# Optimization experiments

Measured on AMD Instinct MI355X. Metric: run time of the kernel, lower is better.

Reference implementation:

```python
import jax, jax.numpy as jnp
import numpy as np

V, E, H, L, T, B = 50257, 1024, 16, 12, 128, 16
FF = 4 * E
STD = 0.02


def setup_inputs() -> dict:
    key = jax.random.key(0)
    ks = jax.random.split(key, 20)
    n = lambda k, shape: (jax.random.normal(k, shape, dtype=jnp.float32) * STD)
    inp = {
        'idx': jax.random.randint(ks[0], (B, T), 0, V, dtype=jnp.int64),
        'targets': jax.random.randint(ks[1], (B, T), 0, V, dtype=jnp.int64),
        'tok_emb': n(ks[2], (V, E)),
        'pos_emb': n(ks[3], (T, E)),
        'wq': n(ks[4], (L, E, E)),
        'wk': n(ks[5], (L, E, E)),
        'wv': n(ks[6], (L, E, E)),
        'w_proj': n(ks[7], (L, E, E)),
        'b_proj': jnp.zeros((L, E), jnp.float32),
        'ln1_g': jnp.ones((L, E), jnp.float32),
        'ln1_b': jnp.zeros((L, E), jnp.float32),
        'ln2_g': jnp.ones((L, E), jnp.float32),
        'ln2_b': jnp.zeros((L, E), jnp.float32),
        'w_fc1': n(ks[8], (L, E, FF)),
        'b_fc1': jnp.zeros((L, FF), jnp.float32),
        'w_fc2': n(ks[9], (L, FF, E)),
        'b_fc2': jnp.zeros((L, E), jnp.float32),
        'lnf_g': jnp.ones((E,), jnp.float32),
        'lnf_b': jnp.zeros((E,), jnp.float32),
        'w_head': n(ks[10], (E, V)),
        'b_head': jnp.zeros((V,), jnp.float32),
    }
    return inp


def _layernorm(x, g, b, eps=1e-5):
    m = x.mean(-1, keepdims=True)
    v = ((x - m) ** 2).mean(-1, keepdims=True)
    return (x - m) / jnp.sqrt(v + eps) * g + b


def _forward(idx, targets, tok_emb, pos_emb, wq, wk, wv, w_proj, b_proj,
             ln1_g, ln1_b, ln2_g, ln2_b, w_fc1, b_fc1, w_fc2, b_fc2,
             lnf_g, lnf_b, w_head, b_head):
    Bb, Tt = idx.shape
    x = tok_emb[idx] + pos_emb[:Tt]  # (B, T, E)
    causal = jnp.tril(jnp.ones((Tt, Tt), dtype=bool))
    scale = E ** (-0.5)  # NOTE: original scales by full n_embd, not head_size

    def block(x, p):
        (wq_l, wk_l, wv_l, wp_l, bp_l, g1, b1, g2, b2, wf1, bf1, wf2, bf2) = p
        h = _layernorm(x, g1, b1)
        q = (h @ wq_l).reshape(Bb, Tt, H, -1)
        k = (h @ wk_l).reshape(Bb, Tt, H, -1)
        v = (h @ wv_l).reshape(Bb, Tt, H, -1)
        sc = jnp.einsum('bthd,bshd->bhts', q, k) * scale
        sc = jnp.where(causal, sc, -jnp.inf)
        att = jax.nn.softmax(sc, axis=-1)
        o = jnp.einsum('bhts,bshd->bthd', att, v).reshape(Bb, Tt, E)
        x = x + o @ wp_l + bp_l
        h2 = _layernorm(x, g2, b2)
        x = x + jax.nn.relu(h2 @ wf1 + bf1) @ wf2 + bf2
        return x, None

    x, _ = jax.lax.scan(block, x, (wq, wk, wv, w_proj, b_proj, ln1_g, ln1_b,
                                   ln2_g, ln2_b, w_fc1, b_fc1, w_fc2, b_fc2))
    x = _layernorm(x, lnf_g, lnf_b)
    logits = x @ w_head + b_head  # (B, T, V)
    logp = jax.nn.log_softmax(logits, axis=-1)
    nll = -jnp.take_along_axis(logp.reshape(Bb * Tt, -1),
                               targets.reshape(-1, 1), axis=1)
    loss = nll.mean()
    return logits, loss


def reference(idx, targets, tok_emb, pos_emb, wq, wk, wv, w_proj, b_proj,
              ln1_g, ln1_b, ln2_g, ln2_b, w_fc1, b_fc1, w_fc2, b_fc2,
              lnf_g, lnf_b, w_head, b_head):
    return _forward(idx, targets, tok_emb, pos_emb, wq, wk, wv, w_proj, b_proj,
                    ln1_g, ln1_b, ln2_g, ln2_b, w_fc1, b_fc1, w_fc2, b_fc2,
                    lnf_g, lnf_b, w_head, b_head)
```

## Files before the change

kernel.cpp:

```cpp
#include <hip/hip_runtime.h>
#include <math.h>

typedef unsigned short u16;
typedef float f32x4 __attribute__((ext_vector_type(4)));
typedef short bf16x8 __attribute__((ext_vector_type(8)));
typedef unsigned short us4 __attribute__((ext_vector_type(4)));

#define DEVI __device__ __forceinline__

DEVI float bf2f(u16 u) { return __uint_as_float(((unsigned int)u) << 16); }
DEVI u16 f2bf(float f) {
    unsigned int u = __float_as_uint(f);
    u += 0x7fffu + ((u >> 16) & 1u);
    return (u16)(u >> 16);
}

__global__ __launch_bounds__(256) void k_embed(const int* __restrict__ idx,
                                               const float* __restrict__ te,
                                               const float* __restrict__ pe,
                                               float* __restrict__ x) {
    int m = blockIdx.x;
    int t = m & 127;
    int tok = idx[m];
    const f32x4* a = (const f32x4*)(te + (long)tok * 1024);
    const f32x4* p = (const f32x4*)(pe + (long)t * 1024);
    f32x4* o = (f32x4*)(x + (long)m * 1024);
    o[threadIdx.x] = a[threadIdx.x] + p[threadIdx.x];
}

__global__ __launch_bounds__(256) void k_ln(const float* __restrict__ x,
                                            const float* __restrict__ g,
                                            const float* __restrict__ b,
                                            u16* __restrict__ out) {
    __shared__ float red[8];
    int tid = threadIdx.x, lane = tid & 63, wid = tid >> 6;
    int r = blockIdx.x;
    f32x4 v = ((const f32x4*)(x + (long)r * 1024))[tid];
    float s = v.x + v.y + v.z + v.w;
#pragma unroll
    for (int o2 = 32; o2; o2 >>= 1) s += __shfl_xor(s, o2);
    if (lane == 0) red[wid] = s;
    __syncthreads();
    float mean = (red[0] + red[1] + red[2] + red[3]) * (1.0f / 1024.0f);
    f32x4 d; d.x = v.x - mean; d.y = v.y - mean; d.z = v.z - mean; d.w = v.w - mean;
    float sq = d.x * d.x + d.y * d.y + d.z * d.z + d.w * d.w;
#pragma unroll
    for (int o2 = 32; o2; o2 >>= 1) sq += __shfl_xor(sq, o2);
    if (lane == 0) red[4 + wid] = sq;
    __syncthreads();
    float rstd = rsqrtf((red[4] + red[5] + red[6] + red[7]) * (1.0f / 1024.0f) + 1e-5f);
    f32x4 gg = ((const f32x4*)g)[tid];
    f32x4 bb = ((const f32x4*)b)[tid];
    us4 o4;
    o4.x = f2bf(d.x * rstd * gg.x + bb.x);
    o4.y = f2bf(d.y * rstd * gg.y + bb.y);
    o4.z = f2bf(d.z * rstd * gg.z + bb.z);
    o4.w = f2bf(d.w * rstd * gg.w + bb.w);
    ((us4*)(out + (long)r * 1024))[tid] = o4;
}

DEVI void tr_tile(const float* __restrict__ in, u16* __restrict__ out,
                  int K, int N, int k0, int n0, int tid, float (*tile)[65]) {
    int trow = tid >> 4;
    int tcol = (tid & 15) * 4;
#pragma unroll
    for (int p = 0; p < 4; ++p) {
        int k = k0 + trow + p * 16;
        const float* src = in + (long)k * N + n0 + tcol;
#pragma unroll
        for (int j = 0; j < 4; ++j) {
            int n = n0 + tcol + j;
            tile[trow + p * 16][tcol + j] = (n < N) ? src[j] : 0.0f;
        }
    }
    __syncthreads();
#pragma unroll
    for (int p = 0; p < 4; ++p) {
        int n = n0 + trow + p * 16;
        if (n < N) {
            us4 o4;
#pragma unroll
            for (int j = 0; j < 4; ++j) o4[j] = f2bf(tile[tcol + j][trow + p * 16]);
            *(us4*)(out + (long)n * K + k0 + tcol) = o4;
        }
    }
}

__global__ __launch_bounds__(256) void k_tr_one(const float* __restrict__ in,
                                                u16* __restrict__ out, int K, int N) {
    __shared__ float tile[64][65];
    tr_tile(in, out, K, N, blockIdx.y * 64, blockIdx.x * 64, threadIdx.x, tile);
}

__global__ __launch_bounds__(256) void k_tr_layer(
    const float* __restrict__ wq, const float* __restrict__ wk,
    const float* __restrict__ wv, const float* __restrict__ wp,
    const float* __restrict__ f1, const float* __restrict__ f2,
    u16* __restrict__ oqkv, u16* __restrict__ oproj,
    u16* __restrict__ of1, u16* __restrict__ of2) {
    __shared__ float tile[64][65];
    int id = blockIdx.x;
    const float* in; u16* out; int K, N, txx, tyy;
    if (id < 1024) {
        int t = id >> 8, s2 = id & 255;
        txx = s2 & 15; tyy = s2 >> 4; K = 1024; N = 1024;
        in = (t == 0) ? wq : (t == 1) ? wk : (t == 2) ? wv : wp;
        out = (t == 3) ? oproj : oqkv + (long)t * 1024 * 1024;
    } else if (id < 2048) {
        int s2 = id - 1024;
        txx = s2 & 63; tyy = s2 >> 6; K = 1024; N = 4096; in = f1; out = of1;
    } else {
        int s2 = id - 2048;
        txx = s2 & 15; tyy = s2 >> 4; K = 4096; N = 1024; in = f2; out = of2;
    }
    tr_tile(in, out, K, N, tyy * 64, txx * 64, threadIdx.x, tile);
}

template <int ROWS>
DEVI void stage_tile(const u16* __restrict__ g, long row0, long rowmax, int ld,
                     int col0, char* lds, int tid) {
    constexpr int NCH = ROWS * 8;
#pragma unroll
    for (int p = 0; p < NCH / 256; ++p) {
        int c = tid + p * 256;
        int row = c >> 3;
        int gslot = c & 7;
        int gdata = gslot ^ (row & 7);
        long gr = row0 + row;
        if (gr > rowmax) gr = rowmax;
        const u16* src = g + gr * (long)ld + col0 + gdata * 8;
        char* dst = lds + ((long)((tid & 192) + p * 256)) * 16;
        __builtin_amdgcn_global_load_lds(
            (const __attribute__((address_space(1))) void*)src,
            (__attribute__((address_space(3))) void*)dst, 16, 0, 0);
    }
}

template <int BN, bool OUT_BF16, bool RELU, bool HAS_BIAS, bool HAS_RES>
__global__ __launch_bounds__(256, 2) void k_gemm(
    const u16* __restrict__ A, const u16* __restrict__ Bt,
    const float* __restrict__ bias, const float* __restrict__ res,
    float* __restrict__ Cf, u16* __restrict__ Cb,
    int M, int N, int K, int ldc) {
    constexpr int NR = BN / 32;
    constexpr int ASZ = 128 * 64 * 2;
    constexpr int BSZ = BN * 64 * 2;
    __shared__ __align__(16) char lds[2 * (ASZ + BSZ)];
    int tid = threadIdx.x, lane = tid & 63, wid = tid >> 6;
    int l15 = lane & 15, l4 = lane >> 4;
    int wr = wid >> 1, wc = wid & 1;
    long m0 = (long)blockIdx.y * 128;
    long n0 = (long)blockIdx.x * BN;
    f32x4 acc[4][NR] = {};
    const int nk = K >> 6;

    stage_tile<128>(A, m0, (long)M - 1, K, 0, lds, tid);
    stage_tile<BN>(Bt, n0, (long)N - 1, K, 0, lds + ASZ, tid);
    int cur = 0;
    for (int kt = 0; kt < nk; ++kt) {
        __syncthreads();
        if (kt + 1 < nk) {
            char* nb = lds + (cur ^ 1) * (ASZ + BSZ);
            stage_tile<128>(A, m0, (long)M - 1, K, (kt + 1) << 6, nb, tid);
            stage_tile<BN>(Bt, n0, (long)N - 1, K, (kt + 1) << 6, nb + ASZ, tid);
        }
        const char* ab = lds + cur * (ASZ + BSZ);
        const char* bb = ab + ASZ;
#pragma unroll
        for (int kh = 0; kh < 2; ++kh) {
            bf16x8 af[4], bfv[NR];
#pragma unroll
            for (int mi = 0; mi < 4; ++mi) {
                int row = wr * 64 + mi * 16 + l15;
                int slot = (kh * 4 + l4) ^ (row & 7);
                af[mi] = *(const bf16x8*)(ab + (row * 8 + slot) * 16);
            }
#pragma unroll
            for (int ni = 0; ni < NR; ++ni) {
                int row = wc * (BN / 2) + ni * 16 + l15;
                int slot = (kh * 4 + l4) ^ (row & 7);
                bfv[ni] = *(const bf16x8*)(bb + (row * 8 + slot) * 16);
            }
#pragma unroll
            for (int mi = 0; mi < 4; ++mi)
#pragma unroll
                for (int ni = 0; ni < NR; ++ni)
                    acc[mi][ni] = __builtin_amdgcn_mfma_f32_16x16x32_bf16(
                        af[mi], bfv[ni], acc[mi][ni], 0, 0, 0);
        }
        cur ^= 1;
    }
#pragma unroll
    for (int ni = 0; ni < NR; ++ni) {
        long n = n0 + wc * (BN / 2) + ni * 16 + l15;
        if (n < N) {
            float bv = HAS_BIAS ? bias[n] : 0.0f;
#pragma unroll
            for (int mi = 0; mi < 4; ++mi) {
#pragma unroll
                for (int j = 0; j < 4; ++j) {
                    long m = m0 + wr * 64 + mi * 16 + l4 * 4 + j;
                    float v = acc[mi][ni][j] + bv;
                    if (HAS_RES) v += res[m * (long)ldc + n];
                    if (RELU) v = fmaxf(v, 0.0f);
                    if (OUT_BF16) Cb[m * (long)ldc + n] = f2bf(v);
                    else Cf[m * (long)ldc + n] = v;
                }
            }
        }
    }
}

__global__ __launch_bounds__(256, 2) void k_head128(
    const u16* __restrict__ A, const u16* __restrict__ Bt,
    const float* __restrict__ bias, float* __restrict__ Cf,
    float2* __restrict__ part, int M, int N, int K, int ldc, int ncb) {
    constexpr int ASZ = 128 * 64 * 2;
    constexpr int BSZ = 128 * 64 * 2;
    __shared__ __align__(16) char lds[2 * (ASZ + BSZ)];
    __shared__ float pmx[2][128], psm[2][128];
    int tid = threadIdx.x, lane = tid & 63, wid = tid >> 6;
    int l15 = lane & 15, l4 = lane >> 4;
    int wr = wid >> 1, wc = wid & 1;
    int bn = blockIdx.x, bm = blockIdx.y;
    long m0 = (long)bm * 128, n0 = (long)bn * 128;
    f32x4 acc[4][4] = {};
    const int nk = K >> 6;

    stage_tile<128>(A, m0, (long)M - 1, K, 0, lds, tid);
    stage_tile<128>(Bt, n0, (long)N - 1, K, 0, lds + ASZ, tid);
    int cur = 0;
    for (int kt = 0; kt < nk; ++kt) {
        __syncthreads();
        if (kt + 1 < nk) {
            char* nb = lds + (cur ^ 1) * (ASZ + BSZ);
            stage_tile<128>(A, m0, (long)M - 1, K, (kt + 1) << 6, nb, tid);
            stage_tile<128>(Bt, n0, (long)N - 1, K, (kt + 1) << 6, nb + ASZ, tid);
        }
        const char* ab = lds + cur * (ASZ + BSZ);
        const char* bb = ab + ASZ;
#pragma unroll
        for (int kh = 0; kh < 2; ++kh) {
            bf16x8 af[4], bfv[4];
#pragma unroll
            for (int mi = 0; mi < 4; ++mi) {
                int row = wr * 64 + mi * 16 + l15;
                int slot = (kh * 4 + l4) ^ (row & 7);
                af[mi] = *(const bf16x8*)(ab + (row * 8 + slot) * 16);
            }
#pragma unroll
            for (int ni = 0; ni < 4; ++ni) {
                int row = wc * 64 + ni * 16 + l15;
                int slot = (kh * 4 + l4) ^ (row & 7);
                bfv[ni] = *(const bf16x8*)(bb + (row * 8 + slot) * 16);
            }
#pragma unroll
            for (int mi = 0; mi < 4; ++mi)
#pragma unroll
                for (int ni = 0; ni < 4; ++ni)
                    acc[mi][ni] = __builtin_amdgcn_mfma_f32_16x16x32_bf16(
                        af[mi], bfv[ni], acc[mi][ni], 0, 0, 0);
        }
        cur ^= 1;
    }
    const float BIG_NEG = -1e30f;
    float bvv[4];
#pragma unroll
    for (int ni = 0; ni < 4; ++ni) {
        long n = n0 + wc * 64 + ni * 16 + l15;
        bvv[ni] = (n < N) ? bias[n] : 0.0f;
    }
#pragma unroll
    for (int mi = 0; mi < 4; ++mi) {
#pragma unroll
        for (int j = 0; j < 4; ++j) {
            int rloc = wr * 64 + mi * 16 + l4 * 4 + j;
            long m = m0 + rloc;
            float mx = BIG_NEG, vv[4];
#pragma unroll
            for (int ni = 0; ni < 4; ++ni) {
                long n = n0 + wc * 64 + ni * 16 + l15;
                float v = acc[mi][ni][j] + bvv[ni];
                if (n < N) Cf[m * (long)ldc + n] = v;
                else v = BIG_NEG;
                vv[ni] = v;
                mx = fmaxf(mx, v);
            }
#pragma unroll
            for (int ofs = 1; ofs < 16; ofs <<= 1) mx = fmaxf(mx, __shfl_xor(mx, ofs));
            float sm = 0.f;
#pragma unroll
            for (int ni = 0; ni < 4; ++ni) sm += __expf(vv[ni] - mx);
#pragma unroll
            for (int ofs = 1; ofs < 16; ofs <<= 1) sm += __shfl_xor(sm, ofs);
            if (l15 == 0) { pmx[wc][rloc] = mx; psm[wc][rloc] = sm; }
        }
    }
    __syncthreads();
    if (tid < 128) {
        float m1 = pmx[0][tid], m2 = pmx[1][tid];
        float nm = fmaxf(m1, m2);
        float S = psm[0][tid] * __expf(m1 - nm) + psm[1][tid] * __expf(m2 - nm);
        part[(m0 + tid) * (long)ncb + bn] = make_float2(nm, S);
    }
}

__global__ __launch_bounds__(256) void k_attn_mfma(const u16* __restrict__ qkv,
                                                   u16* __restrict__ o) {
    __shared__ __align__(16) u16 Ks[128 * 64];
    __shared__ __align__(16) u16 Vt[64 * 128];
    __shared__ __align__(16) u16 Ps[4][32 * 128];
    int tid = threadIdx.x, lane = tid & 63, w = tid >> 6;
    int l15 = lane & 15, l4 = lane >> 4;
    int b = blockIdx.x >> 4, h = blockIdx.x & 15;
    const u16* base = qkv + (long)b * 128 * 3072 + h * 64;

    stage_tile<128>(base + 1024, 0, 127, 3072, 0, (char*)Ks, tid);
    {
        const u16* vg = base + 2048;
#pragma unroll
        for (int p = 0; p < 4; ++p) {
            int s0 = (w * 4 + p) * 8;
            u16 tmp[8];
#pragma unroll
            for (int j = 0; j < 8; ++j) tmp[j] = vg[(long)(s0 + j) * 3072 + lane];
            int slot = (s0 >> 3) ^ (lane & 7);
            *(bf16x8*)((char*)Vt + lane * 256 + slot * 16) = *(bf16x8*)tmp;
        }
    }
    bf16x8 aq[2][2];
#pragma unroll
    for (int mj = 0; mj < 2; ++mj)
#pragma unroll
        for (int kk = 0; kk < 2; ++kk)
            aq[mj][kk] = *(const bf16x8*)(base + (long)(w * 32 + mj * 16 + l15) * 3072 + kk * 32 + l4 * 8);
    __syncthreads();

    f32x4 sacc[2][8] = {};
#pragma unroll
    for (int sj = 0; sj < 8; ++sj) {
        bf16x8 bk[2];
#pragma unroll
        for (int kk = 0; kk < 2; ++kk) {
            int row = sj * 16 + l15;
            int slot = (kk * 4 + l4) ^ (row & 7);
            bk[kk] = *(const bf16x8*)((char*)Ks + (row * 8 + slot) * 16);
        }
#pragma unroll
        for (int mj = 0; mj < 2; ++mj) {
            sacc[mj][sj] = __builtin_amdgcn_mfma_f32_16x16x32_bf16(aq[mj][0], bk[0], sacc[mj][sj], 0, 0, 0);
            sacc[mj][sj] = __builtin_amdgcn_mfma_f32_16x16x32_bf16(aq[mj][1], bk[1], sacc[mj][sj], 0, 0, 0);
        }
    }
    const float scale = 0.03125f;
#pragma unroll
    for (int mj = 0; mj < 2; ++mj) {
#pragma unroll
        for (int j = 0; j < 4; ++j) {
            int tq = w * 32 + mj * 16 + l4 * 4 + j;
            float mx = -INFINITY;
#pragma unroll
            for (int sj = 0; sj < 8; ++sj) {
                int s = sj * 16 + l15;
                float v = (s <= tq) ? sacc[mj][sj][j] * scale : -INFINITY;
                sacc[mj][sj][j] = v;
                mx = fmaxf(mx, v);
            }
#pragma unroll
            for (int ofs = 1; ofs < 16; ofs <<= 1) mx = fmaxf(mx, __shfl_xor(mx, ofs));
            float sm = 0.f;
#pragma unroll
            for (int sj = 0; sj < 8; ++sj) {
                float e = __expf(sacc[mj][sj][j] - mx);
                sacc[mj][sj][j] = e;
                sm += e;
            }
#pragma unroll
            for (int ofs = 1; ofs < 16; ofs <<= 1) sm += __shfl_xor(sm, ofs);
            float inv = 1.0f / sm;
            int m2 = mj * 16 + l4 * 4 + j;
            u16* prow = Ps[w] + m2 * 128;
#pragma unroll
            for (int sj = 0; sj < 8; ++sj) {
                int s = sj * 16 + l15;
                int slot = (s >> 3) ^ (m2 & 7);
                prow[slot * 8 + (s & 7)] = f2bf(sacc[mj][sj][j] * inv);
            }
        }
    }
    f32x4 oacc[2][4] = {};
#pragma unroll
    for (int kk = 0; kk < 4; ++kk) {
        bf16x8 pa[2], bv[4];
#pragma unroll
        for (int mj = 0; mj < 2; ++mj) {
            int m2 = mj * 16 + l15;
            int slot = (kk * 4 + l4) ^ (m2 & 7);
            pa[mj] = *(const bf16x8*)((char*)(Ps[w]) + m2 * 256 + slot * 16);
        }
#pragma unroll
        for (int nb = 0; nb < 4; ++nb) {
            int d = nb * 16 + l15;
            int slot = (kk * 4 + l4) ^ (d & 7);
            bv[nb] = *(const bf16x8*)((char*)Vt + d * 256 + slot * 16);
        }
#pragma unroll
        for (int mj = 0; mj < 2; ++mj)
#pragma unroll
            for (int nb = 0; nb < 4; ++nb)
                oacc[mj][nb] = __builtin_amdgcn_mfma_f32_16x16x32_bf16(pa[mj], bv[nb], oacc[mj][nb], 0, 0, 0);
    }
#pragma unroll
    for (int mj = 0; mj < 2; ++mj)
#pragma unroll
        for (int nb = 0; nb < 4; ++nb) {
            int d = nb * 16 + l15;
#pragma unroll
            for (int j = 0; j < 4; ++j) {
                int tq = w * 32 + mj * 16 + l4 * 4 + j;
                o[((long)b * 128 + tq) * 1024 + h * 64 + d] = f2bf(oacc[mj][nb][j]);
            }
        }
}

__global__ __launch_bounds__(64) void k_loss_rows2(const float2* __restrict__ part,
                                                   const float* __restrict__ logits,
                                                   const int* __restrict__ tgt,
                                                   float* __restrict__ rowloss, int ncb) {
    int r = blockIdx.x, lane = threadIdx.x;
    float M = -1e30f, S = 0.f;
    for (int cb = lane; cb < ncb; cb += 64) {
        float2 p = part[(long)r * ncb + cb];
        float nm = fmaxf(M, p.x);
        S = S * __expf(M - nm) + p.y * __expf(p.x - nm);
        M = nm;
    }
#pragma unroll
    for (int ofs = 32; ofs; ofs >>= 1) {
        float M2 = __shfl_xor(M, ofs), S2 = __shfl_xor(S, ofs);
        float nm = fmaxf(M, M2);
        S = S * __expf(M - nm) + S2 * __expf(M2 - nm);
        M = nm;
    }
    if (lane == 0)
        rowloss[r] = (M + logf(S)) - logits[(long)r * 50257 + tgt[r]];
}

__global__ __launch_bounds__(256) void k_loss_reduce(const float* __restrict__ rowloss,
                                                     float* __restrict__ out) {
    __shared__ float red[4];
    int tid = threadIdx.x, lane = tid & 63, wid = tid >> 6;
    float s = 0.f;
    for (int i = tid; i < 2048; i += 256) s += rowloss[i];
#pragma unroll
    for (int ofs = 32; ofs; ofs >>= 1) s += __shfl_xor(s, ofs);
    if (lane == 0) red[wid] = s;
    __syncthreads();
    if (tid == 0) out[0] = (red[0] + red[1] + red[2] + red[3]) * (1.0f / 2048.0f);
}

extern "C" void kernel_launch(void* const* d_in, const int* in_sizes, int n_in,
                              void* d_out, int out_size, void* d_ws, size_t ws_size,
                              hipStream_t stream) {
    (void)in_sizes; (void)n_in; (void)out_size; (void)ws_size;
    const int*   idx     = (const int*)d_in[0];
    const int*   targets = (const int*)d_in[1];
    const float* tok_emb = (const float*)d_in[2];
    const float* pos_emb = (const float*)d_in[3];
    const float* wq      = (const float*)d_in[4];
    const float* wk      = (const float*)d_in[5];
    const float* wv      = (const float*)d_in[6];
    const float* w_proj  = (const float*)d_in[7];
    const float* b_proj  = (const float*)d_in[8];
    const float* ln1_g   = (const float*)d_in[9];
    const float* ln1_b   = (const float*)d_in[10];
    const float* ln2_g   = (const float*)d_in[11];
    const float* ln2_b   = (const float*)d_in[12];
    const float* w_fc1   = (const float*)d_in[13];
    const float* b_fc1   = (const float*)d_in[14];
    const float* w_fc2   = (const float*)d_in[15];
    const float* b_fc2   = (const float*)d_in[16];
    const float* lnf_g   = (const float*)d_in[17];
    const float* lnf_b   = (const float*)d_in[18];
    const float* w_head  = (const float*)d_in[19];
    const float* b_head  = (const float*)d_in[20];
    float* out = (float*)d_out;

    char* w = (char*)d_ws;
    auto alloc = [&](size_t bytes) {
        char* p = w;
        w += (bytes + 255) & ~(size_t)255;
        return p;
    };
    u16*    wT_qkv  = (u16*)alloc(3072L * 1024 * 2);
    u16*    wT_proj = (u16*)alloc(1024L * 1024 * 2);
    u16*    wT_f1   = (u16*)alloc(4096L * 1024 * 2);
    u16*    wT_f2   = (u16*)alloc(1024L * 4096 * 2);
    u16*    wT_head = (u16*)alloc(50257L * 1024 * 2);
    float*  x       = (float*)alloc(2048L * 1024 * 4);
    u16*    h_bf    = (u16*)alloc(2048L * 1024 * 2);
    u16*    qkvb    = (u16*)alloc(2048L * 3072 * 2);
    u16*    o_bf    = (u16*)alloc(2048L * 1024 * 2);
    u16*    ff_bf   = (u16*)alloc(2048L * 4096 * 2);
    float2* part    = (float2*)alloc(2048L * 393 * 8);
    float*  rowloss = (float*)alloc(2048L * 4);

    k_embed<<<2048, 256, 0, stream>>>(idx, tok_emb, pos_emb, x);
    k_tr_one<<<dim3(786, 16), 256, 0, stream>>>(w_head, wT_head, 1024, 50257);

    for (int l = 0; l < 12; ++l) {
        k_tr_layer<<<3072, 256, 0, stream>>>(
            wq + (long)l * 1048576, wk + (long)l * 1048576,
            wv + (long)l * 1048576, w_proj + (long)l * 1048576,
            w_fc1 + (long)l * 4194304, w_fc2 + (long)l * 4194304,
            wT_qkv, wT_proj, wT_f1, wT_f2);
        k_ln<<<2048, 256, 0, stream>>>(x, ln1_g + l * 1024, ln1_b + l * 1024, h_bf);
        k_gemm<128, true, false, false, false><<<dim3(24, 16), 256, 0, stream>>>(
            h_bf, wT_qkv, nullptr, nullptr, nullptr, qkvb, 2048, 3072, 1024, 3072);
        k_attn_mfma<<<256, 256, 0, stream>>>(qkvb, o_bf);
        k_gemm<64, false, false, true, true><<<dim3(16, 16), 256, 0, stream>>>(
            o_bf, wT_proj, b_proj + l * 1024, x, x, nullptr, 2048, 1024, 1024, 1024);
        k_ln<<<2048, 256, 0, stream>>>(x, ln2_g + l * 1024, ln2_b + l * 1024, h_bf);
        k_gemm<128, true, true, true, false><<<dim3(32, 16), 256, 0, stream>>>(
            h_bf, wT_f1, b_fc1 + l * 4096, nullptr, nullptr, ff_bf, 2048, 4096, 1024, 4096);
        k_gemm<64, false, false, true, true><<<dim3(16, 16), 256, 0, stream>>>(
            ff_bf, wT_f2, b_fc2 + l * 1024, x, x, nullptr, 2048, 1024, 4096, 1024);
    }
    k_ln<<<2048, 256, 0, stream>>>(x, lnf_g, lnf_b, h_bf);
    k_head128<<<dim3(393, 16), 256, 0, stream>>>(h_bf, wT_head, b_head, out, part,
                                                 2048, 50257, 1024, 50257, 393);
    k_loss_rows2<<<2048, 64, 0, stream>>>(part, out, targets, rowloss, 393);
    k_loss_reduce<<<1, 256, 0, stream>>>(rowloss, out + 102926336L);
}
```

Measured before the change: 2.192 ms.

## Stage head logits through LDS for coalesced stores; retune GEMM tiles and occupancy

The LM-head epilogue now writes the accumulator tile into padded LDS, then issues row-contiguous nontemporal global stores and computes per-row max/sum-exp partials from LDS. The partials are stored column-block-major, and the loss kernel reads them in that layout. Separately, the QKV and FC1 GEMMs switch from BN=128 to BN=64 tiles with twice the blocks, and k_gemm launch bounds rise to 3 blocks per SM. These aim to cut uncoalesced 50257-wide logit writes and to raise GEMM occupancy, at the cost of extra LDS traffic, a sync, and possible register pressure.

```diff
diff --git a/kernel.cpp b/kernel.cpp
--- a/kernel.cpp
+++ b/kernel.cpp
@@ -137,7 +137,7 @@
 }
 
 template <int BN, bool OUT_BF16, bool RELU, bool HAS_BIAS, bool HAS_RES>
-__global__ __launch_bounds__(256, 2) void k_gemm(
+__global__ __launch_bounds__(256, 3) void k_gemm(
     const u16* __restrict__ A, const u16* __restrict__ Bt,
     const float* __restrict__ bias, const float* __restrict__ res,
     float* __restrict__ Cf, u16* __restrict__ Cb,
@@ -214,11 +214,10 @@
 __global__ __launch_bounds__(256, 2) void k_head128(
     const u16* __restrict__ A, const u16* __restrict__ Bt,
     const float* __restrict__ bias, float* __restrict__ Cf,
-    float2* __restrict__ part, int M, int N, int K, int ldc, int ncb) {
+    float2* __restrict__ part, int M, int N, int K, int ldc) {
     constexpr int ASZ = 128 * 64 * 2;
     constexpr int BSZ = 128 * 64 * 2;
-    __shared__ __align__(16) char lds[2 * (ASZ + BSZ)];
-    __shared__ float pmx[2][128], psm[2][128];
+    __shared__ __align__(16) char lds[128 * 129 * 4];
     int tid = threadIdx.x, lane = tid & 63, wid = tid >> 6;
     int l15 = lane & 15, l4 = lane >> 4;
     int wr = wid >> 1, wc = wid & 1;
@@ -270,38 +269,45 @@
         long n = n0 + wc * 64 + ni * 16 + l15;
         bvv[ni] = (n < N) ? bias[n] : 0.0f;
     }
-#pragma unroll
-    for (int mi = 0; mi < 4; ++mi) {
-#pragma unroll
-        for (int j = 0; j < 4; ++j) {
-            int rloc = wr * 64 + mi * 16 + l4 * 4 + j;
-            long m = m0 + rloc;
-            float mx = BIG_NEG, vv[4];
-#pragma unroll
-            for (int ni = 0; ni < 4; ++ni) {
-                long n = n0 + wc * 64 + ni * 16 + l15;
+    __syncthreads();
+    float* ldsF = (float*)lds;
+#pragma unroll
+    for (int mi = 0; mi < 4; ++mi)
+#pragma unroll
+        for (int ni = 0; ni < 4; ++ni)
+#pragma unroll
+            for (int j = 0; j < 4; ++j) {
+                int row = wr * 64 + mi * 16 + l4 * 4 + j;
+                int col = wc * 64 + ni * 16 + l15;
+                long n = n0 + col;
                 float v = acc[mi][ni][j] + bvv[ni];
-                if (n < N) Cf[m * (long)ldc + n] = v;
-                else v = BIG_NEG;
-                vv[ni] = v;
-                mx = fmaxf(mx, v);
-            }
-#pragma unroll
-            for (int ofs = 1; ofs < 16; ofs <<= 1) mx = fmaxf(mx, __shfl_xor(mx, ofs));
-            float sm = 0.f;
-#pragma unroll
-            for (int ni = 0; ni < 4; ++ni) sm += __expf(vv[ni] - mx);
-#pragma unroll
-            for (int ofs = 1; ofs < 16; ofs <<= 1) sm += __shfl_xor(sm, ofs);
-            if (l15 == 0) { pmx[wc][rloc] = mx; psm[wc][rloc] = sm; }
-        }
-    }
-    __syncthreads();
-    if (tid < 128) {
-        float m1 = pmx[0][tid], m2 = pmx[1][tid];
-        float nm = fmaxf(m1, m2);
-        float S = psm[0][tid] * __expf(m1 - nm) + psm[1][tid] * __expf(m2 - nm);
-        part[(m0 + tid) * (long)ncb + bn] = make_float2(nm, S);
+                if (n >= N) v = BIG_NEG;
+                ldsF[row * 129 + col] = v;
+            }
+    __syncthreads();
+#pragma unroll 4
+    for (int i = 0; i < 64; ++i) {
+        int flat = tid + (i << 8);
+        int row = flat >> 7, col = flat & 127;
+        long n = n0 + col;
+        if (n < N)
+            __builtin_nontemporal_store(ldsF[row * 129 + col],
+                                        &Cf[(m0 + row) * (long)ldc + n]);
+    }
+    {
+        int r = tid >> 1, half = tid & 1;
+        const float* rp = ldsF + r * 129 + half * 64;
+        float mx = BIG_NEG;
+#pragma unroll 8
+        for (int c = 0; c < 64; ++c) mx = fmaxf(mx, rp[c]);
+        float sm = 0.f;
+#pragma unroll 8
+        for (int c = 0; c < 64; ++c) sm += __expf(rp[c] - mx);
+        float mo = __shfl_xor(mx, 1), so = __shfl_xor(sm, 1);
+        float nm = fmaxf(mx, mo);
+        float S = sm * __expf(mx - nm) + so * __expf(mo - nm);
+        if (half == 0)
+            part[(long)bn * M + m0 + r] = make_float2(nm, S);
     }
 }
 
@@ -430,7 +436,7 @@
     int r = blockIdx.x, lane = threadIdx.x;
     float M = -1e30f, S = 0.f;
     for (int cb = lane; cb < ncb; cb += 64) {
-        float2 p = part[(long)r * ncb + cb];
+        float2 p = part[(long)cb * 2048 + r];
         float nm = fmaxf(M, p.x);
         S = S * __expf(M - nm) + p.y * __expf(p.x - nm);
         M = nm;
@@ -502,7 +508,7 @@
     u16*    qkvb    = (u16*)alloc(2048L * 3072 * 2);
     u16*    o_bf    = (u16*)alloc(2048L * 1024 * 2);
     u16*    ff_bf   = (u16*)alloc(2048L * 4096 * 2);
-    float2* part    = (float2*)alloc(2048L * 393 * 8);
+    float2* part    = (float2*)alloc(393L * 2048 * 8);
     float*  rowloss = (float*)alloc(2048L * 4);
 
     k_embed<<<2048, 256, 0, stream>>>(idx, tok_emb, pos_emb, x);
@@ -515,20 +521,20 @@
             w_fc1 + (long)l * 4194304, w_fc2 + (long)l * 4194304,
             wT_qkv, wT_proj, wT_f1, wT_f2);
         k_ln<<<2048, 256, 0, stream>>>(x, ln1_g + l * 1024, ln1_b + l * 1024, h_bf);
-        k_gemm<128, true, false, false, false><<<dim3(24, 16), 256, 0, stream>>>(
+        k_gemm<64, true, false, false, false><<<dim3(48, 16), 256, 0, stream>>>(
             h_bf, wT_qkv, nullptr, nullptr, nullptr, qkvb, 2048, 3072, 1024, 3072);
         k_attn_mfma<<<256, 256, 0, stream>>>(qkvb, o_bf);
         k_gemm<64, false, false, true, true><<<dim3(16, 16), 256, 0, stream>>>(
             o_bf, wT_proj, b_proj + l * 1024, x, x, nullptr, 2048, 1024, 1024, 1024);
         k_ln<<<2048, 256, 0, stream>>>(x, ln2_g + l * 1024, ln2_b + l * 1024, h_bf);
-        k_gemm<128, true, true, true, false><<<dim3(32, 16), 256, 0, stream>>>(
+        k_gemm<64, true, true, true, false><<<dim3(64, 16), 256, 0, stream>>>(
             h_bf, wT_f1, b_fc1 + l * 4096, nullptr, nullptr, ff_bf, 2048, 4096, 1024, 4096);
         k_gemm<64, false, false, true, true><<<dim3(16, 16), 256, 0, stream>>>(
             ff_bf, wT_f2, b_fc2 + l * 1024, x, x, nullptr, 2048, 1024, 4096, 1024);
     }
     k_ln<<<2048, 256, 0, stream>>>(x, lnf_g, lnf_b, h_bf);
     k_head128<<<dim3(393, 16), 256, 0, stream>>>(h_bf, wT_head, b_head, out, part,
-                                                 2048, 50257, 1024, 50257, 393);
+                                                 2048, 50257, 1024, 50257);
     k_loss_rows2<<<2048, 64, 0, stream>>>(part, out, targets, rowloss, 393);
     k_loss_reduce<<<1, 256, 0, stream>>>(rowloss, out + 102926336L);
 }
```

New measurement: 2.130 ms. 1.03x faster.
